# Kernel optimization log

Measured on AMD Instinct MI355X. Metric: run time of the kernel, lower is better.

Reference implementation:

```python
import jax, jax.numpy as jnp
import numpy as np

USER_NUM = 128          # K: users, also equals RIS elements N due to W_v packing
NOISE_DBM = -80.0       # downlink_noise_power
N0 = 10.0 ** (NOISE_DBM / 10.0) / 1000.0  # = exp(p/10*ln10)/1000


def setup_inputs() -> dict:
    key = jax.random.key(0)
    k1, k2, k3, k4, k5 = jax.random.split(key, 5)
    M, K, N = 1024, USER_NUM, USER_NUM  # antennas, users, RIS elements
    return {
        "W_v": jax.random.normal(k1, (M + 1, 2 * K), dtype=jnp.float32),
        "A_real": jax.random.normal(k2, (K, M, N), dtype=jnp.float32),
        "A_imag": jax.random.normal(k3, (K, M, N), dtype=jnp.float32),
        "h_d_real": jax.random.normal(k4, (K, M), dtype=jnp.float32),
        "h_d_imag": jax.random.normal(k5, (K, M), dtype=jnp.float32),
    }


def reference(W_v, A_real, A_imag, h_d_real, h_d_imag):
    # unpack: row 0 is v (RIS phase vector), rows 1.. are W (beamformers)
    v = W_v[0]            # [2N]
    W = W_v[1:]           # [M, 2K]
    C = W.shape[1] // 2   # = K = user_num = N
    W_re, W_im = W[:, :C], W[:, C:]      # [M, K]
    v_re, v_im = v[:C], v[C:]            # [N]

    # effective channel h_k = h_d[k] + A[k] @ v  (complex product, real arithmetic)
    Av_re = jnp.einsum('kmn,n->km', A_real, v_re) - jnp.einsum('kmn,n->km', A_imag, v_im)
    Av_im = jnp.einsum('kmn,n->km', A_imag, v_re) + jnp.einsum('kmn,n->km', A_real, v_im)
    h_re = h_d_real + Av_re              # [K, M]
    h_im = h_d_imag + Av_im              # [K, M]

    # gamma[k, i] = w_i^T h_k (complex, no conjugate, matching the block-matrix math)
    g_re = h_re @ W_re - h_im @ W_im     # [K, K]
    g_im = h_re @ W_im + h_im @ W_re     # [K, K]
    mag = jnp.sqrt(g_re * g_re + g_im * g_im)  # |gamma| (modulus, NOT squared)

    sig = jnp.diagonal(mag)                       # |w_k^T h_k|
    interf = jnp.sum(mag, axis=1) - sig           # sum_{i != k} |w_i^T h_k|
    R = sig / (interf + N0)                       # per-user 'rate' term
    return (-jnp.sum(R) * 1.0e6)[None]            # shape (1,), matches torch.zeros(1) accumulator
```

## Files before the change

### kernel.cpp

```cpp
#include <hip/hip_runtime.h>


#define NSLICE 16
#define MSL    64

typedef float vf4 __attribute__((ext_vector_type(4)));

__device__ __forceinline__ float dot4v(vf4 a, const float4& b) {
    return a.x*b.x + a.y*b.y + a.z*b.z + a.w*b.w;
}

template<int CTRL>
__device__ __forceinline__ float dpp_xadd(float x) {
    union { float f; int i; } u, v;
    u.f = x;
    v.i = __builtin_amdgcn_mov_dpp(u.i, CTRL, 0xf, 0xf, false);
    return x + v.f;
}

__device__ __forceinline__ float sum16(float x) {
    x = dpp_xadd<0xB1>(x);
    x = dpp_xadd<0x4E>(x);
    x = dpp_xadd<0x141>(x);
    x = dpp_xadd<0x140>(x);
    return x;
}

__global__ __launch_bounds__(256, 4) void fused_hg_kernel(
    const float* __restrict__ A_real,
    const float* __restrict__ A_imag,
    const float* __restrict__ W_v,
    const float* __restrict__ h_d_real,
    const float* __restrict__ h_d_imag,
    float* __restrict__ part_re,
    float* __restrict__ part_im,
    float* __restrict__ out)
{
    const int kp    = blockIdx.x >> 4;
    const int slice = blockIdx.x & 15;
    const int t     = threadIdx.x;
    const int lane  = t & 63;
    const int wv    = t >> 6;
    const int sub   = lane & 15;
    const int rsub  = lane >> 4;
    const int k0 = kp, k1 = kp + 64;

    if (blockIdx.x == 0 && t == 0) *out = 0.f;

    __shared__ float sh_re[2][MSL], sh_im[2][MSL];

    const float4 vr0 = ((const float4*)W_v)[sub];
    const float4 vr1 = ((const float4*)W_v)[sub + 16];
    const float4 vi0 = ((const float4*)W_v)[32 + sub];
    const float4 vi1 = ((const float4*)W_v)[48 + sub];

    #pragma unroll
    for (int it = 0; it < 4; ++it) {
        const int row = (wv * 4 + it) * 8 + rsub;
        const int u   = row >> 6;
        const int ml  = row & 63;
        const int k   = u ? k1 : k0;
        const size_t rb = (size_t)k * 1024 + (size_t)slice * MSL + ml;
        const vf4* Ar0 = (const vf4*)(A_real + rb * 128);
        const vf4* Ai0 = (const vf4*)(A_imag + rb * 128);

        const vf4 a0 = __builtin_nontemporal_load(Ar0 + sub);
        const vf4 a1 = __builtin_nontemporal_load(Ar0 + sub + 16);
        const vf4 b0 = __builtin_nontemporal_load(Ai0 + sub);
        const vf4 b1 = __builtin_nontemporal_load(Ai0 + sub + 16);
        const vf4 c0 = __builtin_nontemporal_load(Ar0 + 128 + sub);
        const vf4 c1 = __builtin_nontemporal_load(Ar0 + 128 + sub + 16);
        const vf4 d0 = __builtin_nontemporal_load(Ai0 + 128 + sub);
        const vf4 d1 = __builtin_nontemporal_load(Ai0 + 128 + sub + 16);

        float p_re = dot4v(a0, vr0) + dot4v(a1, vr1) - dot4v(b0, vi0) - dot4v(b1, vi1);
        float p_im = dot4v(b0, vr0) + dot4v(b1, vr1) + dot4v(a0, vi0) + dot4v(a1, vi1);
        float q_re = dot4v(c0, vr0) + dot4v(c1, vr1) - dot4v(d0, vi0) - dot4v(d1, vi1);
        float q_im = dot4v(d0, vr0) + dot4v(d1, vr1) + dot4v(c0, vi0) + dot4v(c1, vi1);

        p_re = sum16(p_re);
        p_im = sum16(p_im);
        q_re = sum16(q_re);
        q_im = sum16(q_im);

        if (sub == 0) {
            sh_re[u][ml]     = h_d_real[rb]     + p_re;
            sh_im[u][ml]     = h_d_imag[rb]     + p_im;
            sh_re[u][ml + 4] = h_d_real[rb + 4] + q_re;
            sh_im[u][ml + 4] = h_d_imag[rb + 4] + q_im;
        }
    }
    __syncthreads();

    const int c4  = t & 31;
    const int seg = t >> 5;
    const float* Wb = W_v + 256 + (size_t)(slice * MSL) * 256;
    float4 gre0 = {0,0,0,0}, gim0 = {0,0,0,0};
    float4 gre1 = {0,0,0,0}, gim1 = {0,0,0,0};
    const int m0 = seg * 8;
    #pragma unroll
    for (int m = m0; m < m0 + 8; ++m) {
        const float4* Wr4 = (const float4*)(Wb + m * 256);
        float4 wr = Wr4[c4];
        float4 wi = Wr4[c4 + 32];
        float hr0 = sh_re[0][m], hi0 = sh_im[0][m];
        float hr1 = sh_re[1][m], hi1 = sh_im[1][m];
        gre0.x = fmaf(hr0, wr.x, fmaf(-hi0, wi.x, gre0.x));
        gre0.y = fmaf(hr0, wr.y, fmaf(-hi0, wi.y, gre0.y));
        gre0.z = fmaf(hr0, wr.z, fmaf(-hi0, wi.z, gre0.z));
        gre0.w = fmaf(hr0, wr.w, fmaf(-hi0, wi.w, gre0.w));
        gim0.x = fmaf(hr0, wi.x, fmaf(hi0, wr.x, gim0.x));
        gim0.y = fmaf(hr0, wi.y, fmaf(hi0, wr.y, gim0.y));
        gim0.z = fmaf(hr0, wi.z, fmaf(hi0, wr.z, gim0.z));
        gim0.w = fmaf(hr0, wi.w, fmaf(hi0, wr.w, gim0.w));
        gre1.x = fmaf(hr1, wr.x, fmaf(-hi1, wi.x, gre1.x));
        gre1.y = fmaf(hr1, wr.y, fmaf(-hi1, wi.y, gre1.y));
        gre1.z = fmaf(hr1, wr.z, fmaf(-hi1, wi.z, gre1.z));
        gre1.w = fmaf(hr1, wr.w, fmaf(-hi1, wi.w, gre1.w));
        gim1.x = fmaf(hr1, wi.x, fmaf(hi1, wr.x, gim1.x));
        gim1.y = fmaf(hr1, wi.y, fmaf(hi1, wr.y, gim1.y));
        gim1.z = fmaf(hr1, wi.z, fmaf(hi1, wr.z, gim1.z));
        gim1.w = fmaf(hr1, wi.w, fmaf(hi1, wr.w, gim1.w));
    }

    __shared__ float4 s_re[2][256], s_im[2][256];
    s_re[0][t] = gre0; s_im[0][t] = gim0;
    s_re[1][t] = gre1; s_im[1][t] = gim1;
    __syncthreads();
    if (t < 64) {
        const int u  = t >> 5;
        const int cg = t & 31;
        float4 r = s_re[u][cg], i = s_im[u][cg];
        #pragma unroll
        for (int s = 1; s < 8; ++s) {
            float4 rr = s_re[u][s * 32 + cg], ii = s_im[u][s * 32 + cg];
            r.x += rr.x; r.y += rr.y; r.z += rr.z; r.w += rr.w;
            i.x += ii.x; i.y += ii.y; i.z += ii.z; i.w += ii.w;
        }
        const int k = (u == 0) ? k0 : k1;
        float4* pr = (float4*)(part_re + (size_t)(slice * 128 + k) * 128);
        float4* pi = (float4*)(part_im + (size_t)(slice * 128 + k) * 128);
        pr[cg] = r;
        pi[cg] = i;
    }
}

__global__ __launch_bounds__(128) void rate_kernel(
    const float* __restrict__ part_re,
    const float* __restrict__ part_im,
    float* __restrict__ out)
{
    const int k = blockIdx.x;
    const int c = threadIdx.x;

    float gr = 0.f, gi = 0.f;
    #pragma unroll
    for (int s = 0; s < NSLICE; ++s) {
        gr += part_re[(s * 128 + k) * 128 + c];
        gi += part_im[(s * 128 + k) * 128 + c];
    }
    float mag = sqrtf(gr * gr + gi * gi);

    __shared__ float s_sig;
    __shared__ float s_w[2];
    if (c == k) s_sig = mag;

    float v = mag;
    #pragma unroll
    for (int off = 32; off > 0; off >>= 1) v += __shfl_xor(v, off);
    if ((c & 63) == 0) s_w[c >> 6] = v;
    __syncthreads();

    if (c == 0) {
        float total  = s_w[0] + s_w[1];
        float interf = total - s_sig;
        float R      = s_sig / (interf + 1e-11f);
        atomicAdd(out, -R * 1e6f);
    }
}

extern "C" void kernel_launch(void* const* d_in, const int* in_sizes, int n_in,
                              void* d_out, int out_size, void* d_ws, size_t ws_size,
                              hipStream_t stream) {
    const float* W_v      = (const float*)d_in[0];
    const float* A_real   = (const float*)d_in[1];
    const float* A_imag   = (const float*)d_in[2];
    const float* h_d_real = (const float*)d_in[3];
    const float* h_d_imag = (const float*)d_in[4];
    float* out  = (float*)d_out;

    float* part_re = (float*)d_ws;
    float* part_im = part_re + NSLICE * 128 * 128;

    fused_hg_kernel<<<1024, 256, 0, stream>>>(A_real, A_imag, W_v,
                                              h_d_real, h_d_imag,
                                              part_re, part_im, out);
    rate_kernel<<<128, 128, 0, stream>>>(part_re, part_im, out);
}
```

Before: 154.0 us.

## Software-pipeline A loads and transpose partial layout for rate reduction

The A-row streaming loop now prefetches the next iteration's eight vector loads before computing on the current ones, so memory latency overlaps the dot products and DPP reductions. The partial-sum buffer is reordered to be k-major so each rate block reads contiguous slices. The rate kernel uses 256 threads and splits the slice sum across two halves combined through shared memory. Prefetching doubles live vector registers, which may hurt occupancy under the 4-blocks launch bound. The compiler may already have hoisted these loads in the fully unrolled loop.

```diff
diff --git a/kernel.cpp b/kernel.cpp
--- a/kernel.cpp
+++ b/kernel.cpp
@@ -54,40 +54,66 @@
     const float4 vi0 = ((const float4*)W_v)[32 + sub];
     const float4 vi1 = ((const float4*)W_v)[48 + sub];
 
-    #pragma unroll
-    for (int it = 0; it < 4; ++it) {
-        const int row = (wv * 4 + it) * 8 + rsub;
-        const int u   = row >> 6;
-        const int ml  = row & 63;
-        const int k   = u ? k1 : k0;
-        const size_t rb = (size_t)k * 1024 + (size_t)slice * MSL + ml;
-        const vf4* Ar0 = (const vf4*)(A_real + rb * 128);
-        const vf4* Ai0 = (const vf4*)(A_imag + rb * 128);
-
-        const vf4 a0 = __builtin_nontemporal_load(Ar0 + sub);
-        const vf4 a1 = __builtin_nontemporal_load(Ar0 + sub + 16);
-        const vf4 b0 = __builtin_nontemporal_load(Ai0 + sub);
-        const vf4 b1 = __builtin_nontemporal_load(Ai0 + sub + 16);
-        const vf4 c0 = __builtin_nontemporal_load(Ar0 + 128 + sub);
-        const vf4 c1 = __builtin_nontemporal_load(Ar0 + 128 + sub + 16);
-        const vf4 d0 = __builtin_nontemporal_load(Ai0 + 128 + sub);
-        const vf4 d1 = __builtin_nontemporal_load(Ai0 + 128 + sub + 16);
-
-        float p_re = dot4v(a0, vr0) + dot4v(a1, vr1) - dot4v(b0, vi0) - dot4v(b1, vi1);
-        float p_im = dot4v(b0, vr0) + dot4v(b1, vr1) + dot4v(a0, vi0) + dot4v(a1, vi1);
-        float q_re = dot4v(c0, vr0) + dot4v(c1, vr1) - dot4v(d0, vi0) - dot4v(d1, vi1);
-        float q_im = dot4v(d0, vr0) + dot4v(d1, vr1) + dot4v(c0, vi0) + dot4v(c1, vi1);
-
-        p_re = sum16(p_re);
-        p_im = sum16(p_im);
-        q_re = sum16(q_re);
-        q_im = sum16(q_im);
-
-        if (sub == 0) {
-            sh_re[u][ml]     = h_d_real[rb]     + p_re;
-            sh_im[u][ml]     = h_d_imag[rb]     + p_im;
-            sh_re[u][ml + 4] = h_d_real[rb + 4] + q_re;
-            sh_im[u][ml + 4] = h_d_imag[rb + 4] + q_im;
+    const int row0 = wv * 32 + rsub;
+    {
+        int row = row0;
+        int u = row >> 6, ml = row & 63;
+        size_t rb = (size_t)(u ? k1 : k0) * 1024 + (size_t)slice * MSL + ml;
+        const vf4* Ar = (const vf4*)(A_real + rb * 128);
+        const vf4* Ai = (const vf4*)(A_imag + rb * 128);
+        vf4 a0 = __builtin_nontemporal_load(Ar + sub);
+        vf4 a1 = __builtin_nontemporal_load(Ar + sub + 16);
+        vf4 b0 = __builtin_nontemporal_load(Ai + sub);
+        vf4 b1 = __builtin_nontemporal_load(Ai + sub + 16);
+        vf4 c0 = __builtin_nontemporal_load(Ar + 128 + sub);
+        vf4 c1 = __builtin_nontemporal_load(Ar + 128 + sub + 16);
+        vf4 d0 = __builtin_nontemporal_load(Ai + 128 + sub);
+        vf4 d1 = __builtin_nontemporal_load(Ai + 128 + sub + 16);
+
+        #pragma unroll
+        for (int it = 0; it < 4; ++it) {
+            row = row0 + it * 8;
+            u = row >> 6; ml = row & 63;
+            rb = (size_t)(u ? k1 : k0) * 1024 + (size_t)slice * MSL + ml;
+
+            vf4 na0, na1, nb0, nb1, nc0, nc1, nd0, nd1;
+            if (it < 3) {
+                const int nrow = row + 8;
+                const int nu = nrow >> 6, nml = nrow & 63;
+                const size_t nrb = (size_t)(nu ? k1 : k0) * 1024 + (size_t)slice * MSL + nml;
+                const vf4* nAr = (const vf4*)(A_real + nrb * 128);
+                const vf4* nAi = (const vf4*)(A_imag + nrb * 128);
+                na0 = __builtin_nontemporal_load(nAr + sub);
+                na1 = __builtin_nontemporal_load(nAr + sub + 16);
+                nb0 = __builtin_nontemporal_load(nAi + sub);
+                nb1 = __builtin_nontemporal_load(nAi + sub + 16);
+                nc0 = __builtin_nontemporal_load(nAr + 128 + sub);
+                nc1 = __builtin_nontemporal_load(nAr + 128 + sub + 16);
+                nd0 = __builtin_nontemporal_load(nAi + 128 + sub);
+                nd1 = __builtin_nontemporal_load(nAi + 128 + sub + 16);
+            }
+
+            float p_re = dot4v(a0, vr0) + dot4v(a1, vr1) - dot4v(b0, vi0) - dot4v(b1, vi1);
+            float p_im = dot4v(b0, vr0) + dot4v(b1, vr1) + dot4v(a0, vi0) + dot4v(a1, vi1);
+            float q_re = dot4v(c0, vr0) + dot4v(c1, vr1) - dot4v(d0, vi0) - dot4v(d1, vi1);
+            float q_im = dot4v(d0, vr0) + dot4v(d1, vr1) + dot4v(c0, vi0) + dot4v(c1, vi1);
+
+            p_re = sum16(p_re);
+            p_im = sum16(p_im);
+            q_re = sum16(q_re);
+            q_im = sum16(q_im);
+
+            if (sub == 0) {
+                sh_re[u][ml]     = h_d_real[rb]     + p_re;
+                sh_im[u][ml]     = h_d_imag[rb]     + p_im;
+                sh_re[u][ml + 4] = h_d_real[rb + 4] + q_re;
+                sh_im[u][ml + 4] = h_d_imag[rb + 4] + q_im;
+            }
+
+            if (it < 3) {
+                a0 = na0; a1 = na1; b0 = nb0; b1 = nb1;
+                c0 = nc0; c1 = nc1; d0 = nd0; d1 = nd1;
+            }
         }
     }
     __syncthreads();
@@ -138,40 +164,52 @@
             i.x += ii.x; i.y += ii.y; i.z += ii.z; i.w += ii.w;
         }
         const int k = (u == 0) ? k0 : k1;
-        float4* pr = (float4*)(part_re + (size_t)(slice * 128 + k) * 128);
-        float4* pi = (float4*)(part_im + (size_t)(slice * 128 + k) * 128);
+        float4* pr = (float4*)(part_re + ((size_t)k * NSLICE + slice) * 128);
+        float4* pi = (float4*)(part_im + ((size_t)k * NSLICE + slice) * 128);
         pr[cg] = r;
         pi[cg] = i;
     }
 }
 
-__global__ __launch_bounds__(128) void rate_kernel(
+__global__ __launch_bounds__(256) void rate_kernel(
     const float* __restrict__ part_re,
     const float* __restrict__ part_im,
     float* __restrict__ out)
 {
-    const int k = blockIdx.x;
-    const int c = threadIdx.x;
+    const int k    = blockIdx.x;
+    const int t    = threadIdx.x;
+    const int c    = t & 127;
+    const int half = t >> 7;
+
+    const float* br = part_re + (size_t)k * (NSLICE * 128);
+    const float* bi = part_im + (size_t)k * (NSLICE * 128);
 
     float gr = 0.f, gi = 0.f;
     #pragma unroll
-    for (int s = 0; s < NSLICE; ++s) {
-        gr += part_re[(s * 128 + k) * 128 + c];
-        gi += part_im[(s * 128 + k) * 128 + c];
-    }
-    float mag = sqrtf(gr * gr + gi * gi);
+    for (int s = half * 8; s < half * 8 + 8; ++s) {
+        gr += br[s * 128 + c];
+        gi += bi[s * 128 + c];
+    }
+
+    __shared__ float rr[256], ri[256];
+    rr[t] = gr; ri[t] = gi;
+    __syncthreads();
 
     __shared__ float s_sig;
     __shared__ float s_w[2];
-    if (c == k) s_sig = mag;
-
-    float v = mag;
-    #pragma unroll
-    for (int off = 32; off > 0; off >>= 1) v += __shfl_xor(v, off);
-    if ((c & 63) == 0) s_w[c >> 6] = v;
-    __syncthreads();
-
-    if (c == 0) {
+    if (t < 128) {
+        gr = rr[t] + rr[t + 128];
+        gi = ri[t] + ri[t + 128];
+        float mag = sqrtf(gr * gr + gi * gi);
+        if (c == k) s_sig = mag;
+        float v = mag;
+        #pragma unroll
+        for (int off = 32; off > 0; off >>= 1) v += __shfl_xor(v, off);
+        if ((c & 63) == 0) s_w[c >> 6] = v;
+    }
+    __syncthreads();
+
+    if (t == 0) {
         float total  = s_w[0] + s_w[1];
         float interf = total - s_sig;
         float R      = s_sig / (interf + 1e-11f);
@@ -190,10 +228,10 @@
     float* out  = (float*)d_out;
 
     float* part_re = (float*)d_ws;
-    float* part_im = part_re + NSLICE * 128 * 128;
+    float* part_im = part_re + 128 * NSLICE * 128;
 
     fused_hg_kernel<<<1024, 256, 0, stream>>>(A_real, A_imag, W_v,
                                               h_d_real, h_d_imag,
                                               part_re, part_im, out);
-    rate_kernel<<<128, 128, 0, stream>>>(part_re, part_im, out);
-}
+    rate_kernel<<<128, 256, 0, stream>>>(part_re, part_im, out);
+}
```

Measured after the change: 157.2 us. 1.02x slower.
